# Performance work log

Measured on AMD Instinct MI355X. Metric: run time of the kernel, lower is better.

## Reference

```python
import jax, jax.numpy as jnp
import numpy as np

RADIUS = 8.0   # matches init kwarg radius
EPS = 1e-8     # nn.CosineSimilarity eps


def _denorm(p, height, width):
    # kornia denormalize_pixel_coordinates: [-1,1] -> [0, size-1]
    scale = jnp.array([(width - 1) * 0.5, (height - 1) * 0.5], dtype=p.dtype)
    return (p + 1.0) * scale


def setup_inputs() -> dict:
    key = jax.random.key(0)
    k1, k2, k3, k4 = jax.random.split(key, 4)
    B, N, D = 4, 2048, 256
    features = jax.random.normal(k1, (B, N, D), dtype=jnp.float32)
    pts_src = jax.random.uniform(k2, (B, N, 2), dtype=jnp.float32) * 2.0 - 1.0
    pts_dst = jax.random.uniform(k3, (B, B, N, 2), dtype=jnp.float32) * 2.0 - 1.0
    invis_idx = jax.random.randint(k4, (3, 128), 0, N)
    return {"features": features, "pts_src": pts_src, "pts_dst": pts_dst,
            "invis_idx": invis_idx, "height": 480, "width": 640}


def reference(features, pts_src, pts_dst, invis_idx, height, width):
    # features: [B,N,D]; pts_src: [B,N,2]; pts_dst: [B,B,N,2]
    B, N, D = features.shape
    ps = _denorm(jax.lax.stop_gradient(pts_src), height, width)   # [B,N,2]
    pd = _denorm(jax.lax.stop_gradient(pts_dst), height, width)   # [B,B,N,2]

    # squared euclidean distance d2[i,j,n,m] = ||ps[i,n] - pd[i,j,m]||^2
    s_src = jnp.sum(ps * ps, axis=-1)          # [B,N]
    s_dst = jnp.sum(pd * pd, axis=-1)          # [B,B,N]
    cross = jnp.einsum('ind,ijmd->ijnm', ps, pd)
    d2 = s_src[:, None, :, None] + s_dst[:, :, None, :] - 2.0 * cross  # [B,B,N,N]
    mask = d2 <= RADIUS * RADIUS

    # pair p = i*B + j of the flattened [B^2] grid matches src batch j (p % B)
    # with dst batch i (p // B):
    # cos[i,j,n,m] = <features[j,n], features[i,m]> / max(|f_jn|*|f_im|, eps)
    dots = jnp.einsum('jnd,imd->ijnm', features, features)  # [B,B,N,N]
    norms = jnp.sqrt(jnp.sum(features * features, axis=-1))  # [B,N]
    denom = jnp.maximum(norms[None, :, :, None] * norms[:, None, None, :], EPS)
    cos = dots / denom

    cnt = jnp.maximum(jnp.sum(mask), 1).astype(features.dtype)
    return jnp.sum(jnp.where(mask, 1.0 - cos, 0.0)) / cnt
```

## Files before the change

### kernel.cpp

```cpp
#include <hip/hip_runtime.h>

#define BB 4
#define NN 2048
#define DD 256
#define TILE_N 32
#define NPW 8
#define NT (NN / TILE_N)
#define MSPLIT 2
#define MLEN (NN / MSPLIT)
#define MCH (MLEN / 128)
#define WQ_CAP 96
#define NBLK (BB * BB * NT * MSPLIT)

__global__ __launch_bounds__(256) void scan_kernel(const float* __restrict__ feat,
                                                   const float* __restrict__ pts_src,
                                                   const float* __restrict__ pts_dst,
                                                   const int* __restrict__ hptr,
                                                   const int* __restrict__ wptr,
                                                   float* __restrict__ psum,
                                                   unsigned int* __restrict__ pcnt) {
    __shared__ unsigned int wq[4][WQ_CAP];
    __shared__ unsigned int wqc[4];
    __shared__ float bsum[4];
    __shared__ unsigned int bcnt[4];
    const int pair  = blockIdx.x >> 7;
    const int tile  = (blockIdx.x >> 1) & (NT - 1);
    const int mhalf = blockIdx.x & 1;
    const int mbase = mhalf * MLEN;
    const int i = pair >> 2;
    const int j = pair & 3;
    const float sx = ((float)(*wptr) - 1.0f) * 0.5f;
    const float sy = ((float)(*hptr) - 1.0f) * 0.5f;

    const int wave = threadIdx.x >> 6;
    const int lane = threadIdx.x & 63;
    if (lane == 0) wqc[wave] = 0u;

    const int nbase = tile * TILE_N + wave * NPW;
    float psx[NPW], psy[NPW];
#pragma unroll
    for (int k = 0; k < NPW; ++k) {
        psx[k] = fmaf(pts_src[(size_t)(i * NN + nbase + k) * 2 + 0], sx, sx);
        psy[k] = fmaf(pts_src[(size_t)(i * NN + nbase + k) * 2 + 1], sy, sy);
    }

    const float4* pd = (const float4*)(pts_dst + (size_t)pair * NN * 2 + (size_t)mbase * 2);

    float4 q = pd[lane];
#pragma unroll
    for (int c = 0; c < MCH; ++c) {
        float4 qn;
        if (c + 1 < MCH) qn = pd[(c + 1) * 64 + lane];
        const float qx0 = fmaf(q.x, sx, sx), qy0 = fmaf(q.y, sy, sy);
        const float qx1 = fmaf(q.z, sx, sx), qy1 = fmaf(q.w, sy, sy);
        float mn = 1e30f;
#pragma unroll
        for (int k = 0; k < NPW; ++k) {
            const float ax = psx[k] - qx0, ay = psy[k] - qy0;
            const float bx = psx[k] - qx1, by = psy[k] - qy1;
            mn = fminf(mn, fminf(fmaf(ax, ax, ay * ay), fmaf(bx, bx, by * by)));
        }
        if (__ballot(mn <= 64.0f)) {
            const unsigned int m2 = (unsigned int)(mbase + c * 128 + 2 * lane);
#pragma unroll
            for (int k = 0; k < NPW; ++k) {
                const float ax = psx[k] - qx0, ay = psy[k] - qy0;
                const float bx = psx[k] - qx1, by = psy[k] - qy1;
                const float d0 = fmaf(ax, ax, ay * ay);
                const float d1 = fmaf(bx, bx, by * by);
                if (fminf(d0, d1) <= 64.0f) {
                    if (d0 <= 64.0f) {
                        const unsigned int slot = atomicAdd(&wqc[wave], 1u);
                        if (slot < WQ_CAP) wq[wave][slot] = ((unsigned int)k << 11) | m2;
                    }
                    if (d1 <= 64.0f) {
                        const unsigned int slot = atomicAdd(&wqc[wave], 1u);
                        if (slot < WQ_CAP) wq[wave][slot] = ((unsigned int)k << 11) | (m2 + 1u);
                    }
                }
            }
        }
        q = qn;
    }

    const unsigned int hc = min(wqc[wave], (unsigned int)WQ_CAP);
    const int g = lane >> 2, sub = lane & 3;
    float lsum = 0.0f;
    for (unsigned int h0 = 0; h0 < hc; h0 += 16) {
        const unsigned int hid = h0 + (unsigned int)g;
        const bool valid = hid < hc;
        float dd = 0.0f, aa = 0.0f, bb = 0.0f;
        if (valid) {
            const unsigned int rec = wq[wave][hid];
            const int m = (int)(rec & 2047u);
            const int n = nbase + (int)(rec >> 11);
            const float4* pa = (const float4*)(feat + (size_t)(j * NN + n) * DD);
            const float4* pb = (const float4*)(feat + (size_t)(i * NN + m) * DD);
#pragma unroll
            for (int t = 0; t < 16; ++t) {
                const float4 a = pa[t * 4 + sub];
                const float4 b = pb[t * 4 + sub];
                dd = fmaf(a.x, b.x, fmaf(a.y, b.y, fmaf(a.z, b.z, fmaf(a.w, b.w, dd))));
                aa = fmaf(a.x, a.x, fmaf(a.y, a.y, fmaf(a.z, a.z, fmaf(a.w, a.w, aa))));
                bb = fmaf(b.x, b.x, fmaf(b.y, b.y, fmaf(b.z, b.z, fmaf(b.w, b.w, bb))));
            }
        }
        dd += __shfl_xor(dd, 1, 64);  aa += __shfl_xor(aa, 1, 64);  bb += __shfl_xor(bb, 1, 64);
        dd += __shfl_xor(dd, 2, 64);  aa += __shfl_xor(aa, 2, 64);  bb += __shfl_xor(bb, 2, 64);
        if (valid && sub == 0) {
            const float p = aa * bb;
            float r = rsqrtf(p);
            r = r * (1.5f - 0.5f * p * r * r);
            lsum += 1.0f - dd * r;
        }
    }
#pragma unroll
    for (int off = 32; off >= 1; off >>= 1) lsum += __shfl_xor(lsum, off, 64);

    if (lane == 0) { bsum[wave] = lsum; bcnt[wave] = hc; }
    __syncthreads();
    if (threadIdx.x == 0) {
        psum[blockIdx.x] = bsum[0] + bsum[1] + bsum[2] + bsum[3];
        pcnt[blockIdx.x] = bcnt[0] + bcnt[1] + bcnt[2] + bcnt[3];
    }
}

__global__ __launch_bounds__(256) void finalize_kernel(const float* __restrict__ psum,
                                                       const unsigned int* __restrict__ pcnt,
                                                       float* __restrict__ out) {
    float s = 0.0f;
    float c = 0.0f;
    for (int t = threadIdx.x; t < NBLK; t += 256) {
        s += psum[t];
        c += (float)pcnt[t];
    }
#pragma unroll
    for (int off = 32; off >= 1; off >>= 1) {
        s += __shfl_xor(s, off, 64);
        c += __shfl_xor(c, off, 64);
    }
    __shared__ float ss[4], cc[4];
    const int wave = threadIdx.x >> 6;
    const int lane = threadIdx.x & 63;
    if (lane == 0) { ss[wave] = s; cc[wave] = c; }
    __syncthreads();
    if (threadIdx.x == 0) {
        const float S = ss[0] + ss[1] + ss[2] + ss[3];
        const float C = cc[0] + cc[1] + cc[2] + cc[3];
        out[0] = S / fmaxf(C, 1.0f);
    }
}

extern "C" void kernel_launch(void* const* d_in, const int* in_sizes, int n_in,
                              void* d_out, int out_size, void* d_ws, size_t ws_size,
                              hipStream_t stream) {
    const float* feat    = (const float*)d_in[0];
    const float* pts_src = (const float*)d_in[1];
    const float* pts_dst = (const float*)d_in[2];
    const int* hptr = (const int*)d_in[4];
    const int* wptr = (const int*)d_in[5];
    float* out = (float*)d_out;

    float*        psum  = (float*)d_ws;
    unsigned int* pcnt  = (unsigned int*)((char*)d_ws + 8192);

    scan_kernel<<<NBLK, 256, 0, stream>>>(feat, pts_src, pts_dst,
                                          hptr, wptr, psum, pcnt);
    finalize_kernel<<<1, 256, 0, stream>>>(psum, pcnt, out);
}
```

Measured before the change: 86.80 us.

## Drop M-split, remap blocks across XCDs, widen per-hit lane groups

Each block now scans the full 2048 destination points instead of half, which halves the grid and the per-block setup and partial reductions. Blocks are remapped so consecutive block indices spread pairs across the 8 XCDs, aiming for better L2 locality of pts_dst and features. The cosine stage uses 8 lanes per hit instead of 4 with a shorter inner loop, the queue capacity grows to 128, and the launch bounds and chunk-loop unroll are adjusted. Each block now does twice the scan work, so there is less parallelism to hide latency.

```diff
diff --git a/kernel.cpp b/kernel.cpp
--- a/kernel.cpp
+++ b/kernel.cpp
@@ -6,27 +6,27 @@
 #define TILE_N 32
 #define NPW 8
 #define NT (NN / TILE_N)
-#define MSPLIT 2
-#define MLEN (NN / MSPLIT)
+#define MLEN NN
 #define MCH (MLEN / 128)
-#define WQ_CAP 96
-#define NBLK (BB * BB * NT * MSPLIT)
+#define WQ_CAP 128
+#define NBLK (BB * BB * NT)
 
-__global__ __launch_bounds__(256) void scan_kernel(const float* __restrict__ feat,
-                                                   const float* __restrict__ pts_src,
-                                                   const float* __restrict__ pts_dst,
-                                                   const int* __restrict__ hptr,
-                                                   const int* __restrict__ wptr,
-                                                   float* __restrict__ psum,
-                                                   unsigned int* __restrict__ pcnt) {
+__global__ __launch_bounds__(256, 4) void scan_kernel(const float* __restrict__ feat,
+                                                      const float* __restrict__ pts_src,
+                                                      const float* __restrict__ pts_dst,
+                                                      const int* __restrict__ hptr,
+                                                      const int* __restrict__ wptr,
+                                                      float* __restrict__ psum,
+                                                      unsigned int* __restrict__ pcnt) {
     __shared__ unsigned int wq[4][WQ_CAP];
     __shared__ unsigned int wqc[4];
     __shared__ float bsum[4];
     __shared__ unsigned int bcnt[4];
-    const int pair  = blockIdx.x >> 7;
-    const int tile  = (blockIdx.x >> 1) & (NT - 1);
-    const int mhalf = blockIdx.x & 1;
-    const int mbase = mhalf * MLEN;
+
+    const int xcd  = blockIdx.x & 7;
+    const int slot = blockIdx.x >> 3;
+    const int pair = xcd | ((slot >> 6) << 3);
+    const int tile = slot & 63;
     const int i = pair >> 2;
     const int j = pair & 3;
     const float sx = ((float)(*wptr) - 1.0f) * 0.5f;
@@ -44,10 +44,10 @@
         psy[k] = fmaf(pts_src[(size_t)(i * NN + nbase + k) * 2 + 1], sy, sy);
     }
 
-    const float4* pd = (const float4*)(pts_dst + (size_t)pair * NN * 2 + (size_t)mbase * 2);
+    const float4* pd = (const float4*)(pts_dst + (size_t)pair * NN * 2);
 
     float4 q = pd[lane];
-#pragma unroll
+#pragma unroll 4
     for (int c = 0; c < MCH; ++c) {
         float4 qn;
         if (c + 1 < MCH) qn = pd[(c + 1) * 64 + lane];
@@ -61,7 +61,7 @@
             mn = fminf(mn, fminf(fmaf(ax, ax, ay * ay), fmaf(bx, bx, by * by)));
         }
         if (__ballot(mn <= 64.0f)) {
-            const unsigned int m2 = (unsigned int)(mbase + c * 128 + 2 * lane);
+            const unsigned int m2 = (unsigned int)(c * 128 + 2 * lane);
 #pragma unroll
             for (int k = 0; k < NPW; ++k) {
                 const float ax = psx[k] - qx0, ay = psy[k] - qy0;
@@ -70,12 +70,12 @@
                 const float d1 = fmaf(bx, bx, by * by);
                 if (fminf(d0, d1) <= 64.0f) {
                     if (d0 <= 64.0f) {
-                        const unsigned int slot = atomicAdd(&wqc[wave], 1u);
-                        if (slot < WQ_CAP) wq[wave][slot] = ((unsigned int)k << 11) | m2;
+                        const unsigned int slot2 = atomicAdd(&wqc[wave], 1u);
+                        if (slot2 < WQ_CAP) wq[wave][slot2] = ((unsigned int)k << 11) | m2;
                     }
                     if (d1 <= 64.0f) {
-                        const unsigned int slot = atomicAdd(&wqc[wave], 1u);
-                        if (slot < WQ_CAP) wq[wave][slot] = ((unsigned int)k << 11) | (m2 + 1u);
+                        const unsigned int slot2 = atomicAdd(&wqc[wave], 1u);
+                        if (slot2 < WQ_CAP) wq[wave][slot2] = ((unsigned int)k << 11) | (m2 + 1u);
                     }
                 }
             }
@@ -84,9 +84,9 @@
     }
 
     const unsigned int hc = min(wqc[wave], (unsigned int)WQ_CAP);
-    const int g = lane >> 2, sub = lane & 3;
+    const int g = lane >> 3, sub = lane & 7;
     float lsum = 0.0f;
-    for (unsigned int h0 = 0; h0 < hc; h0 += 16) {
+    for (unsigned int h0 = 0; h0 < hc; h0 += 8) {
         const unsigned int hid = h0 + (unsigned int)g;
         const bool valid = hid < hc;
         float dd = 0.0f, aa = 0.0f, bb = 0.0f;
@@ -97,9 +97,9 @@
             const float4* pa = (const float4*)(feat + (size_t)(j * NN + n) * DD);
             const float4* pb = (const float4*)(feat + (size_t)(i * NN + m) * DD);
 #pragma unroll
-            for (int t = 0; t < 16; ++t) {
-                const float4 a = pa[t * 4 + sub];
-                const float4 b = pb[t * 4 + sub];
+            for (int t = 0; t < 8; ++t) {
+                const float4 a = pa[t * 8 + sub];
+                const float4 b = pb[t * 8 + sub];
                 dd = fmaf(a.x, b.x, fmaf(a.y, b.y, fmaf(a.z, b.z, fmaf(a.w, b.w, dd))));
                 aa = fmaf(a.x, a.x, fmaf(a.y, a.y, fmaf(a.z, a.z, fmaf(a.w, a.w, aa))));
                 bb = fmaf(b.x, b.x, fmaf(b.y, b.y, fmaf(b.z, b.z, fmaf(b.w, b.w, bb))));
@@ -107,6 +107,7 @@
         }
         dd += __shfl_xor(dd, 1, 64);  aa += __shfl_xor(aa, 1, 64);  bb += __shfl_xor(bb, 1, 64);
         dd += __shfl_xor(dd, 2, 64);  aa += __shfl_xor(aa, 2, 64);  bb += __shfl_xor(bb, 2, 64);
+        dd += __shfl_xor(dd, 4, 64);  aa += __shfl_xor(aa, 4, 64);  bb += __shfl_xor(bb, 4, 64);
         if (valid && sub == 0) {
             const float p = aa * bb;
             float r = rsqrtf(p);
```

Result: slower. 88.71 us (+2.2%).
